# Kernel tuning notes

Hardware: AMD Instinct MI355X
Metric: run time of the kernel (lower is better)

Reference implementation:

```python
import jax, jax.numpy as jnp
import numpy as np

V = 8000      # output_size (vocab)
EMB = 256     # emb_size
ENC = 512     # enc_hid_size
DEC = 512     # dec_hid_size
HE = 20       # energizer hidden (fixed in source)


def setup_inputs() -> dict:
    key = jax.random.key(0)
    ks = jax.random.split(key, 12)
    B, S, T = 64, 128, 128
    s = 0.05
    return {
        "enc_hid": jax.random.normal(ks[0], (B, S, ENC), dtype=jnp.float32),
        "real_output": jax.random.randint(ks[1], (B, T), 0, V),
        "W_e1": jax.random.normal(ks[2], (ENC + DEC, HE), dtype=jnp.float32) * s,
        "b_e1": jnp.zeros((HE,), jnp.float32),
        "W_e2": jax.random.normal(ks[3], (HE, 1), dtype=jnp.float32) * s,
        "b_e2": jnp.zeros((1,), jnp.float32),
        "emb": jax.random.normal(ks[4], (V, EMB), dtype=jnp.float32) * s,
        "W_rnn": jax.random.normal(ks[5], (EMB + DEC + ENC, DEC), dtype=jnp.float32) * s,
        "b_rnn": jnp.zeros((DEC,), jnp.float32),
        "W_out": jax.random.normal(ks[6], (EMB + DEC + ENC, V), dtype=jnp.float32) * s,
        "b_out": jnp.zeros((V,), jnp.float32),
    }


def _decode(enc_hid, real_output, W_e1, b_e1, W_e2, b_e2, emb, W_rnn, b_rnn, W_out, b_out):
    B, S, _ = enc_hid.shape

    def step(carry, y_i):
        last_char, last_hidden = carry  # [B] int, [B,DEC]
        # additive attention, vectorized over all encoder positions
        hid_b = jnp.broadcast_to(last_hidden[:, None, :], (B, S, DEC))
        cat = jnp.concatenate([enc_hid, hid_b], axis=-1)          # [B,S,ENC+DEC]
        e = jax.nn.elu(cat @ W_e1 + b_e1)                          # [B,S,HE]
        e = jax.nn.elu(e @ W_e2 + b_e2)[..., 0]                    # [B,S]
        ew = jnp.exp(e)
        w = ew / jnp.sum(ew, axis=1, keepdims=True)                # [B,S]
        context = jnp.einsum('bs,bse->be', w, enc_hid)             # [B,ENC]
        last_ch = emb[last_char % V]                               # [B,EMB]
        new_hidden = jax.nn.elu(
            jnp.concatenate([last_ch, last_hidden, context], axis=1) @ W_rnn + b_rnn)
        out = jax.nn.elu(
            jnp.concatenate([last_ch, new_hidden, context], axis=1) @ W_out + b_out)
        # teacher_forcing_prob = 1.0 -> next char is the ground truth token
        return (y_i, new_hidden), (out, w)

    init = (jnp.zeros((B,), real_output.dtype), jnp.zeros((B, DEC), enc_hid.dtype))
    _, (outs, weights) = jax.lax.scan(step, init, real_output.T)   # [T,B,V], [T,B,S]
    return outs.transpose(1, 0, 2), weights.transpose(1, 0, 2)


def reference(enc_hid, real_output, W_e1, b_e1, W_e2, b_e2, emb, W_rnn, b_rnn, W_out, b_out):
    return _decode(enc_hid, real_output, W_e1, b_e1, W_e2, b_e2, emb,
                   W_rnn, b_rnn, W_out, b_out)
```

## Files before the change

kernel.cpp:

```cpp
#include <hip/hip_runtime.h>
#include <hip/hip_bf16.h>
#include <stdint.h>

#define BATCH 64
#define SLEN 128
#define TLEN 128
#define ENCD 512
#define DECD 512
#define EMBD 256
#define VOC  8000
#define HE   20
#define KX   1280
#define NPAD 8064

typedef __attribute__((ext_vector_type(8))) short short8;
typedef __attribute__((ext_vector_type(8))) _Float16 half8v;
typedef __attribute__((ext_vector_type(4))) float f32x4;
typedef _Float16 h2 __attribute__((ext_vector_type(2)));

__device__ inline unsigned short f2bf(float f) {
  union { float f; uint32_t u; } v; v.f = f;
  uint32_t r = v.u + 0x7fff + ((v.u >> 16) & 1);
  return (unsigned short)(r >> 16);
}
__device__ inline unsigned short f16bits(float f) {
  union { _Float16 h; unsigned short u; } c; c.h = (_Float16)f; return c.u;
}
__device__ inline uint32_t pkh2(float a, float b) {
  union { h2 h; uint32_t u; } v;
  v.h = h2{(_Float16)a, (_Float16)b};
  return v.u;
}
__device__ inline float fdot2(uint32_t a, uint32_t b, float c) {
#if __has_builtin(__builtin_amdgcn_fdot2)
  union { uint32_t u; h2 h; } x, y; x.u = a; y.u = b;
  return __builtin_amdgcn_fdot2(x.h, y.h, c, false);
#else
  union { uint32_t u; h2 h; } x, y; x.u = a; y.u = b;
  return c + (float)x.h[0] * (float)y.h[0] + (float)x.h[1] * (float)y.h[1];
#endif
}
__device__ inline float eluf(float x) { return x > 0.f ? x : (expf(x) - 1.f); }

typedef const __attribute__((address_space(1))) unsigned int* gptr_t;
typedef __attribute__((address_space(3))) unsigned int* lptr_t;
__device__ inline void gload16(const void* g, void* l) {
  __builtin_amdgcn_global_load_lds((gptr_t)g, (lptr_t)l, 16, 0, 0);
}

__global__ __launch_bounds__(256) void k_e1(const float* __restrict__ enc,
                                            const float* __restrict__ We1,
                                            float* __restrict__ E1) {
  __shared__ float rowbuf[4][ENCD];
  __shared__ float part[4][HE][2];
  int r0 = blockIdx.x * 4;
  int tid = threadIdx.x;
  for (int i = tid; i < 4 * ENCD; i += 256) {
    int rl = i >> 9, e = i & 511;
    rowbuf[rl][e] = enc[(size_t)(r0 + rl) * ENCD + e];
  }
  __syncthreads();
  if (tid < 160) {
    int kg = tid / 80, rem = tid % 80, rl = rem / 20, h = rem % 20;
    float acc = 0.f;
    for (int k = kg * 256; k < kg * 256 + 256; ++k)
      acc += rowbuf[rl][k] * We1[k * HE + h];
    part[rl][h][kg] = acc;
  }
  __syncthreads();
  if (tid < 80) {
    int rl = tid / 20, h = tid % 20;
    int r = r0 + rl, bb = r >> 7, ss = r & 127;
    E1[((size_t)bb * HE + h) * SLEN + ss] = part[rl][h][0] + part[rl][h][1];
  }
}

__global__ __launch_bounds__(256) void k_tr_wout(const float* __restrict__ Wo,
                                                 unsigned short* __restrict__ WoT) {
  __shared__ float tile[64][65];
  int n0 = blockIdx.x * 64, k0 = blockIdx.y * 64;
  int tid = threadIdx.x;
  for (int i = tid; i < 4096; i += 256) {
    int kk = i >> 6, nn = i & 63;
    int n = n0 + nn;
    tile[kk][nn] = (n < VOC) ? Wo[(size_t)(k0 + kk) * VOC + n] : 0.f;
  }
  __syncthreads();
  for (int i = tid; i < 4096; i += 256) {
    int nn = i >> 6, kk = i & 63;
    WoT[(size_t)(n0 + nn) * KX + k0 + kk] = f2bf(tile[kk][nn]);
  }
}

__global__ __launch_bounds__(256) void k_tr_w(const float* __restrict__ src,
                                              unsigned short* __restrict__ dst,
                                              int k0, int KN, int fmt) {
  __shared__ float tile[64][65];
  int n0 = blockIdx.x * 64, kt = blockIdx.y * 64;
  int tid = threadIdx.x;
  for (int i = tid; i < 4096; i += 256) {
    int kk = i >> 6, nn = i & 63;
    tile[kk][nn] = src[(size_t)(k0 + kt + kk) * 512 + n0 + nn];
  }
  __syncthreads();
  for (int i = tid; i < 4096; i += 256) {
    int nn = i >> 6, kk = i & 63;
    float v = tile[kk][nn];
    dst[(size_t)(n0 + nn) * KN + kt + kk] = fmt ? f2bf(v) : f16bits(v);
  }
}

__global__ __launch_bounds__(256) void k_prep_wr(const float* __restrict__ Wr,
                                                 unsigned short* __restrict__ W2) {
  int i = blockIdx.x * 256 + threadIdx.x;
  int n = i & 511;
  int j = (i >> 9) & 7;
  int kc = (i >> 12) & 31;
  int h = (i >> 17) & 1;
  int k = h * 256 + kc * 8 + j;
  W2[(((size_t)(h * 32 + kc) * 512) + n) * 8 + j] = f16bits(Wr[(size_t)(256 + k) * 512 + n]);
}

__global__ __launch_bounds__(256) void k_ench(const float* __restrict__ enc,
                                              unsigned short* __restrict__ ench) {
  int i = (blockIdx.x * 256 + threadIdx.x) * 4;
  float4 v = *(const float4*)(enc + i);
  ushort4 o = { f16bits(v.x), f16bits(v.y), f16bits(v.z), f16bits(v.w) };
  *(ushort4*)(ench + i) = o;
}

__global__ __launch_bounds__(256) void k_wh(const float* __restrict__ wout,
                                            unsigned short* __restrict__ wh) {
  int i = (blockIdx.x * 256 + threadIdx.x) * 4;
  float4 v = *(const float4*)(wout + i);
  ushort4 o = { f16bits(v.x), f16bits(v.y), f16bits(v.z), f16bits(v.w) };
  *(ushort4*)(wh + i) = o;
}

__global__ __launch_bounds__(256) void k_tr_encb(const float* __restrict__ enc,
                                                 unsigned short* __restrict__ encT) {
  __shared__ float tile[64][65];
  int b = blockIdx.x, e0 = blockIdx.y * 64, s0 = blockIdx.z * 64;
  int tid = threadIdx.x;
  const float* eb = enc + (size_t)b * SLEN * ENCD;
  for (int i = tid; i < 4096; i += 256) {
    int ss = i >> 6, ee = i & 63;
    tile[ss][ee] = eb[(size_t)(s0 + ss) * ENCD + e0 + ee];
  }
  __syncthreads();
  unsigned short* ob = encT + (size_t)b * ENCD * SLEN;
  for (int i = tid; i < 4096; i += 256) {
    int ee = i >> 6, ss = i & 63;
    ob[(size_t)(e0 + ee) * SLEN + s0 + ss] = f16bits(tile[ss][ee]);
  }
}

__global__ __launch_bounds__(256) void k_lc(const int* __restrict__ ro,
                                            const float* __restrict__ emb,
                                            unsigned short* __restrict__ X) {
  int r = blockIdx.x;
  int t = r >> 6, b = r & 63;
  int lc = (t == 0) ? 0 : ro[b * TLEN + t - 1];
  lc = ((lc % VOC) + VOC) % VOC;
  X[(size_t)r * KX + threadIdx.x] = f2bf(emb[(size_t)lc * EMBD + threadIdx.x]);
}

#define BM 128
#define BN 128
#define BK 64

template<int MODE>
__global__ __launch_bounds__(256) void k_gs(
    const unsigned short* __restrict__ A,
    const unsigned short* __restrict__ B,
    const float* __restrict__ bias,
    unsigned short* __restrict__ Cout)
{
  constexpr int As = (MODE == 0) ? KX : (MODE == 1 ? 512 : 128);
  constexpr int Bs = (MODE == 0) ? 256 : (MODE == 1 ? 512 : 128);
  constexpr int KT = (MODE == 0) ? 4 : (MODE == 1 ? 8 : 2);
  __shared__ __align__(16) unsigned short Asd[BM * BK];
  __shared__ __align__(16) unsigned short Bsd[BN * BK];
  int bx = blockIdx.x, by = blockIdx.y;
  int tid = threadIdx.x;
  int wid = tid >> 6, lane = tid & 63;
  int wr = wid >> 1, wc = wid & 1;

  f32x4 acc[4][4];
  for (int i = 0; i < 4; ++i)
    for (int j = 0; j < 4; ++j) acc[i][j] = (f32x4)0.f;

  const unsigned short* Abase = A + (size_t)by * BM * As;
  const unsigned short* Bbase = B + (size_t)bx * BN * Bs + (MODE == 2 ? (size_t)by * 512 * 128 : 0);

  for (int kt = 0; kt < KT; ++kt) {
    for (int j = 0; j < 4; ++j) {
      int c = tid + j * 256;
      int r = c >> 3, c16 = c & 7;
      int sk = c16 ^ (r & 7);
      gload16(Abase + (size_t)r * As + kt * BK + sk * 8, (char*)Asd + c * 16);
      gload16(Bbase + (size_t)r * Bs + kt * BK + sk * 8, (char*)Bsd + c * 16);
    }
    __syncthreads();
    for (int ks = 0; ks < 2; ++ks) {
      short8 af[4], bf[4];
      int kc = ks * 4 + (lane >> 4);
      for (int i = 0; i < 4; ++i) {
        int r = wr * 64 + i * 16 + (lane & 15);
        af[i] = *(const short8*)((const char*)Asd + r * 128 + ((kc ^ (r & 7)) * 16));
      }
      for (int j = 0; j < 4; ++j) {
        int r = wc * 64 + j * 16 + (lane & 15);
        bf[j] = *(const short8*)((const char*)Bsd + r * 128 + ((kc ^ (r & 7)) * 16));
      }
      for (int i = 0; i < 4; ++i)
        for (int j = 0; j < 4; ++j) {
          if constexpr (MODE == 0)
            acc[i][j] = __builtin_amdgcn_mfma_f32_16x16x32_bf16(af[i], bf[j], acc[i][j], 0, 0, 0);
          else
            acc[i][j] = __builtin_amdgcn_mfma_f32_16x16x32_f16(
                __builtin_bit_cast(half8v, af[i]), __builtin_bit_cast(half8v, bf[j]), acc[i][j], 0, 0, 0);
        }
    }
    __syncthreads();
  }

  int rl = lane >> 4, cl = lane & 15;
  for (int j = 0; j < 4; ++j) {
    int gn = bx * BN + wc * 64 + j * 16 + cl;
    for (int i = 0; i < 4; ++i) {
      for (int q = 0; q < 4; ++q) {
        int gm = by * BM + wr * 64 + i * 16 + rl * 4 + q;
        float v = acc[i][j][q];
        if constexpr (MODE == 0) {
          Cout[(size_t)gm * 512 + gn] = f16bits(v + bias[gn]);
        } else if constexpr (MODE == 1) {
          int bb = gm >> 7, s = gm & 127;
          Cout[(((size_t)(bb * 16 + (s >> 3)) * 512) + gn) * 8 + (s & 7)] = f16bits(v);
        } else {
          int tt = gm & 127, bb = gm >> 7;
          Cout[((size_t)tt * 64 + bb) * KX + 768 + gn] = f2bf(v);
        }
      }
    }
  }
}

#define STREAM4(PH) { \
  float a0 = 0, a1 = 0, a2 = 0, a3 = 0; \
  uint4 cb[8], nb[8]; \
  _Pragma("unroll") \
  for (int j = 0; j < 8; ++j) cb[j] = Wp[(size_t)j * 512]; \
  for (int blk = 0; blk < 4; ++blk) { \
    if (blk + 1 < 4) { \
      _Pragma("unroll") \
      for (int j = 0; j < 8; ++j) nb[j] = Wp[(size_t)((blk + 1) * 8 + j) * 512]; \
    } \
    _Pragma("unroll") \
    for (int j = 0; j < 8; ++j) { \
      uint4 wv = cb[j]; uint4 xv = hp4[hbase + blk * 8 + j]; \
      a0 = fdot2(wv.x, xv.x, a0); a1 = fdot2(wv.y, xv.y, a1); \
      a2 = fdot2(wv.z, xv.z, a2); a3 = fdot2(wv.w, xv.w, a3); \
    } \
    _Pragma("unroll") \
    for (int j = 0; j < 8; ++j) cb[j] = nb[j]; \
  } \
  ph[PH][mn] = (a0 + a1) + (a2 + a3); }

__global__ __launch_bounds__(1024) void k_recur(
    const float* __restrict__ We1,
    const float* __restrict__ be1,
    const float* __restrict__ We2,
    const float* __restrict__ be2,
    const uint4* __restrict__ W2,
    const uint4* __restrict__ encW2,
    const unsigned short* __restrict__ Remb,
    const float* __restrict__ E1g,
    unsigned short* __restrict__ X,
    float* __restrict__ wout)
{
  __shared__ __align__(16) uint4 el[16][512];
  __shared__ uint32_t E1p[HE][SLEN / 2];
  __shared__ uint32_t w1p[HE][257];
  __shared__ uint32_t hpair[DECD / 2];
  __shared__ uint32_t wpairS[SLEN / 2];
  __shared__ float ph[2][DECD];
  __shared__ float be1s[HE], w2s[HE];
  __shared__ float be2s;

  int b = blockIdx.x, tid = threadIdx.x;

  for (int i = tid; i < 16 * 512; i += 1024) ((uint4*)el)[i] = encW2[(size_t)b * 8192 + i];
  for (int i = tid; i < HE * (SLEN / 2); i += 1024) {
    int h = i >> 6, p = i & 63;
    const float* ebase = E1g + ((size_t)b * HE + h) * SLEN;
    ((uint32_t*)E1p)[i] = pkh2(ebase[2 * p], ebase[2 * p + 1]);
  }
  for (int i = tid; i < HE * 256; i += 1024) {
    int h = i >> 8, p = i & 255;
    w1p[h][p] = pkh2(We1[(size_t)(ENCD + 2 * p) * HE + h],
                     We1[(size_t)(ENCD + 2 * p + 1) * HE + h]);
  }
  for (int i = tid; i < DECD / 2; i += 1024) hpair[i] = 0;
  for (int i = tid; i < DECD; i += 1024) { ph[0][i] = 0.f; ph[1][i] = 0.f; }
  if (tid < HE) { be1s[tid] = be1[tid]; w2s[tid] = We2[tid]; }
  if (tid == 0) be2s = be2[0];
  __syncthreads();

  const int lane = tid & 63;
  const int wv_ = tid >> 6;
  int mn, mh0;
  if (tid < 448)      { mn = tid;        mh0 = 0; }
  else if (tid < 896) { mn = tid - 448;  mh0 = 1; }
  else if (tid < 960) { mn = 448 + lane; mh0 = 0; }
  else                { mn = 448 + lane; mh0 = 1; }
  const uint4* Wp = W2 + (size_t)(mh0 * 32) * 512 + mn;
  const uint4* hp4 = (const uint4*)hpair;
  const int hbase = mh0 * 32;

  int ah = lane % 20, aseg = lane / 20;
  int q0 = aseg * 86;
  int q1 = (aseg == 2) ? 256 : q0 + 86;
  if (aseg >= 3) { q0 = 0; q1 = 0; }

  for (int t = 0; t < TLEN; ++t) {
    const int rowr = t * BATCH + b;
    float rpre = 0.f;

    if (wv_ < 15) {
      if (tid < 512) {
        union { unsigned short u; _Float16 f; } c;
        c.u = Remb[(size_t)rowr * 512 + tid];
        rpre = (float)c.f;
      }
      STREAM4(mh0)
    } else {
      __builtin_amdgcn_s_setprio(1);
      float p0 = 0, p1 = 0;
      for (int q = q0; q < q1; q += 2) {
        p0 = fdot2(w1p[ah][q], hpair[q], p0);
        p1 = fdot2(w1p[ah][q + 1], hpair[q + 1], p1);
      }
      float p = p0 + p1;
      float pa = __shfl(p, lane + 20);
      float pb = __shfl(p, lane + 40);
      float edv = p + pa + pb + ((lane < HE) ? be1s[lane] : 0.f);
      float e0a = 0.f, e1a = 0.f;
      #pragma unroll
      for (int h = 0; h < HE; ++h) {
        union { uint32_t u; h2 hh; } e; e.u = E1p[h][lane];
        float ed = __shfl(edv, h);
        e0a += eluf((float)e.hh[0] + ed) * w2s[h];
        e1a += eluf((float)e.hh[1] + ed) * w2s[h];
      }
      float s0 = expf(eluf(e0a + be2s));
      float s1 = expf(eluf(e1a + be2s));
      float tot = s0 + s1;
      #pragma unroll
      for (int o = 1; o < 64; o <<= 1) tot += __shfl_xor(tot, o);
      float inv = 1.f / tot;
      float w0 = s0 * inv, w1 = s1 * inv;
      wpairS[lane] = pkh2(w0, w1);
      float2 wv2 = { w0, w1 };
      *(float2*)(wout + ((size_t)b * TLEN + t) * SLEN + 2 * lane) = wv2;
      __builtin_amdgcn_s_setprio(0);
      STREAM4(1)
    }
    __syncthreads();

    if (tid < 512) {
      int n = tid;
      float c0 = 0, c1 = 0, c2 = 0, c3 = 0;
      #pragma unroll
      for (int g = 0; g < 16; ++g) {
        uint4 ev = el[g][n];
        uint4 wv = ((const uint4*)wpairS)[g];
        c0 = fdot2(ev.x, wv.x, c0); c1 = fdot2(ev.y, wv.y, c1);
        c2 = fdot2(ev.z, wv.z, c2); c3 = fdot2(ev.w, wv.w, c3);
      }
      float v = rpre + ph[0][n] + ph[1][n] + (c0 + c1) + (c2 + c3);
      float aa = eluf(v);
      X[(size_t)rowr * KX + 256 + n] = f2bf(aa);
      float bb = __shfl_down(aa, 1);
      if (!(n & 1)) hpair[n >> 1] = pkh2(aa, bb);
    }
    __syncthreads();
  }
}

__global__ __launch_bounds__(256) void k_gemm(
    const unsigned short* __restrict__ Xb,
    const unsigned short* __restrict__ WoT,
    const float* __restrict__ bout,
    float* __restrict__ out)
{
  __shared__ __align__(16) unsigned short As[BM * BK];
  __shared__ __align__(16) unsigned short Bs[BN * BK];
  int bid = blockIdx.x;
  int swz = (bid & 7) * 504 + (bid >> 3);
  int bx = swz % 63;
  int by = swz / 63;
  int tid = threadIdx.x;
  int wid = tid >> 6, lane = tid & 63;
  int wr = wid >> 1, wc = wid & 1;

  f32x4 acc[4][4];
  for (int i = 0; i < 4; ++i)
    for (int j = 0; j < 4; ++j) acc[i][j] = (f32x4)0.f;

  const unsigned short* Abase = Xb + (size_t)by * BM * KX;
  const unsigned short* Bbase = WoT + (size_t)bx * BN * KX;

  for (int kt = 0; kt < KX / BK; ++kt) {
    for (int j = 0; j < 4; ++j) {
      int c = tid + j * 256;
      int r = c >> 3, c16 = c & 7;
      int sk = c16 ^ (r & 7);
      gload16(Abase + (size_t)r * KX + kt * BK + sk * 8, (char*)As + c * 16);
      gload16(Bbase + (size_t)r * KX + kt * BK + sk * 8, (char*)Bs + c * 16);
    }
    __syncthreads();
    for (int ks = 0; ks < 2; ++ks) {
      short8 af[4], bf[4];
      int kc = ks * 4 + (lane >> 4);
      for (int i = 0; i < 4; ++i) {
        int r = wr * 64 + i * 16 + (lane & 15);
        af[i] = *(const short8*)((const char*)As + r * 128 + ((kc ^ (r & 7)) * 16));
      }
      for (int j = 0; j < 4; ++j) {
        int r = wc * 64 + j * 16 + (lane & 15);
        bf[j] = *(const short8*)((const char*)Bs + r * 128 + ((kc ^ (r & 7)) * 16));
      }
      for (int i = 0; i < 4; ++i)
        for (int j = 0; j < 4; ++j)
          acc[i][j] = __builtin_amdgcn_mfma_f32_16x16x32_bf16(af[i], bf[j], acc[i][j], 0, 0, 0);
    }
    __syncthreads();
  }

  int rl = lane >> 4, cl = lane & 15;
  for (int j = 0; j < 4; ++j) {
    int gn = bx * BN + wc * 64 + j * 16 + cl;
    if (gn >= VOC) continue;
    float bv = bout[gn];
    for (int i = 0; i < 4; ++i) {
      for (int q = 0; q < 4; ++q) {
        int gm = by * BM + wr * 64 + i * 16 + rl * 4 + q;
        int tt = gm >> 6, bb = gm & 63;
        float v = acc[i][j][q] + bv;
        v = v > 0.f ? v : (expf(v) - 1.f);
        out[((size_t)bb * TLEN + tt) * VOC + gn] = v;
      }
    }
  }
}

extern "C" void kernel_launch(void* const* d_in, const int* in_sizes, int n_in,
                              void* d_out, int out_size, void* d_ws, size_t ws_size,
                              hipStream_t stream) {
  const float* enc  = (const float*)d_in[0];
  const int*   ro   = (const int*)d_in[1];
  const float* We1  = (const float*)d_in[2];
  const float* be1  = (const float*)d_in[3];
  const float* We2  = (const float*)d_in[4];
  const float* be2  = (const float*)d_in[5];
  const float* emb  = (const float*)d_in[6];
  const float* Wr   = (const float*)d_in[7];
  const float* brnn = (const float*)d_in[8];
  const float* Wo   = (const float*)d_in[9];
  const float* bo   = (const float*)d_in[10];

  char* ws = (char*)d_ws;
  unsigned short* X     = (unsigned short*)(ws);
  unsigned short* WoT   = (unsigned short*)(ws + 20971520);
  unsigned short* W2    = (unsigned short*)(ws + 41615360);
  unsigned short* WembT = (unsigned short*)(ws + 42139648);
  unsigned short* WctxT = (unsigned short*)(ws + 42401792);
  unsigned short* ench  = (unsigned short*)(ws + 42926080);
  float*          E1    = (float*)(ws + 51314688);
  unsigned short* Remb  = (unsigned short*)(ws + 51970048);
  unsigned short* encW2 = (unsigned short*)(ws + 60358656);
  unsigned short* encTh = ench;
  unsigned short* wh    = Remb;

  float* outs = (float*)d_out;
  float* wout = (float*)d_out + (size_t)BATCH * TLEN * VOC;

  k_lc     <<<dim3(8192),     256, 0, stream>>>(ro, emb, X);
  k_e1     <<<dim3(2048),     256, 0, stream>>>(enc, We1, E1);
  k_tr_wout<<<dim3(126, 20),  256, 0, stream>>>(Wo, WoT);
  k_tr_w   <<<dim3(8, 4),     256, 0, stream>>>(Wr, WembT, 0, 256, 1);
  k_tr_w   <<<dim3(8, 8),     256, 0, stream>>>(Wr, WctxT, 768, 512, 0);
  k_prep_wr<<<dim3(1024),     256, 0, stream>>>(Wr, W2);
  k_ench   <<<dim3(4096),     256, 0, stream>>>(enc, ench);
  k_gs<0>  <<<dim3(4, 64),    256, 0, stream>>>(X, WembT, brnn, Remb);
  k_gs<1>  <<<dim3(4, 64),    256, 0, stream>>>(ench, WctxT, brnn, encW2);
  k_recur  <<<dim3(64),      1024, 0, stream>>>(We1, be1, We2, be2,
                                                (const uint4*)W2, (const uint4*)encW2,
                                                Remb, E1, X, wout);
  k_wh     <<<dim3(1024),     256, 0, stream>>>(wout, wh);
  k_tr_encb<<<dim3(64, 8, 2), 256, 0, stream>>>(enc, encTh);
  k_gs<2>  <<<dim3(4, 64),    256, 0, stream>>>(wh, encTh, brnn, X);
  k_gemm   <<<dim3(4032),     256, 0, stream>>>(X, WoT, bo, outs);
  (void)in_sizes; (void)n_in; (void)out_size; (void)ws_size;
}
```

Before: 1.307 ms.

## Fuse prep kernels and overlap weight transposes with recurrent kernel blocks

The small preprocessing kernels are merged into two launches that branch on block index: embedding gather, encoder fp16 conversion and E1 in one, and the W_rnn transposes and repacks in the other. The W_out transpose and the encoder transpose no longer run as separate kernels. They now run in extra blocks of the recurrent kernel, which otherwise keeps only 64 workgroups busy on a GPU with many idle CUs, so this work overlaps the serial recurrence instead of adding to the critical path. The cost is a larger recurrent grid that may contend with the 64 recurrence blocks for memory bandwidth. It also relies on those 64 blocks being dispatched first.

After: 1.256 ms. 1.04x faster.

```diff
diff --git a/kernel.cpp b/kernel.cpp
--- a/kernel.cpp
+++ b/kernel.cpp
@@ -48,85 +48,81 @@
   __builtin_amdgcn_global_load_lds((gptr_t)g, (lptr_t)l, 16, 0, 0);
 }
 
-__global__ __launch_bounds__(256) void k_e1(const float* __restrict__ enc,
-                                            const float* __restrict__ We1,
-                                            float* __restrict__ E1) {
+__global__ __launch_bounds__(256) void k_pre1(const int* __restrict__ ro,
+                                              const float* __restrict__ emb,
+                                              unsigned short* __restrict__ X,
+                                              const float* __restrict__ enc,
+                                              unsigned short* __restrict__ ench,
+                                              const float* __restrict__ We1,
+                                              float* __restrict__ E1) {
   __shared__ float rowbuf[4][ENCD];
   __shared__ float part[4][HE][2];
-  int r0 = blockIdx.x * 4;
-  int tid = threadIdx.x;
-  for (int i = tid; i < 4 * ENCD; i += 256) {
-    int rl = i >> 9, e = i & 511;
-    rowbuf[rl][e] = enc[(size_t)(r0 + rl) * ENCD + e];
-  }
-  __syncthreads();
-  if (tid < 160) {
-    int kg = tid / 80, rem = tid % 80, rl = rem / 20, h = rem % 20;
-    float acc = 0.f;
-    for (int k = kg * 256; k < kg * 256 + 256; ++k)
-      acc += rowbuf[rl][k] * We1[k * HE + h];
-    part[rl][h][kg] = acc;
-  }
-  __syncthreads();
-  if (tid < 80) {
-    int rl = tid / 20, h = tid % 20;
-    int r = r0 + rl, bb = r >> 7, ss = r & 127;
-    E1[((size_t)bb * HE + h) * SLEN + ss] = part[rl][h][0] + part[rl][h][1];
-  }
-}
-
-__global__ __launch_bounds__(256) void k_tr_wout(const float* __restrict__ Wo,
-                                                 unsigned short* __restrict__ WoT) {
+  int bid = blockIdx.x, tid = threadIdx.x;
+  if (bid < 8192) {
+    int r = bid;
+    int t = r >> 6, b = r & 63;
+    int lc = (t == 0) ? 0 : ro[b * TLEN + t - 1];
+    lc = ((lc % VOC) + VOC) % VOC;
+    X[(size_t)r * KX + tid] = f2bf(emb[(size_t)lc * EMBD + tid]);
+  } else if (bid < 12288) {
+    int i = ((bid - 8192) * 256 + tid) * 4;
+    float4 v = *(const float4*)(enc + i);
+    ushort4 o = { f16bits(v.x), f16bits(v.y), f16bits(v.z), f16bits(v.w) };
+    *(ushort4*)(ench + i) = o;
+  } else {
+    int r0 = (bid - 12288) * 4;
+    for (int i = tid; i < 4 * ENCD; i += 256) {
+      int rl = i >> 9, e = i & 511;
+      rowbuf[rl][e] = enc[(size_t)(r0 + rl) * ENCD + e];
+    }
+    __syncthreads();
+    if (tid < 160) {
+      int kg = tid / 80, rem = tid % 80, rl = rem / 20, h = rem % 20;
+      float acc = 0.f;
+      for (int k = kg * 256; k < kg * 256 + 256; ++k)
+        acc += rowbuf[rl][k] * We1[k * HE + h];
+      part[rl][h][kg] = acc;
+    }
+    __syncthreads();
+    if (tid < 80) {
+      int rl = tid / 20, h = tid % 20;
+      int r = r0 + rl, bb = r >> 7, ss = r & 127;
+      E1[((size_t)bb * HE + h) * SLEN + ss] = part[rl][h][0] + part[rl][h][1];
+    }
+  }
+}
+
+__global__ __launch_bounds__(256) void k_pre2(const float* __restrict__ Wr,
+                                              unsigned short* __restrict__ WembT,
+                                              unsigned short* __restrict__ WctxT,
+                                              unsigned short* __restrict__ W2) {
   __shared__ float tile[64][65];
-  int n0 = blockIdx.x * 64, k0 = blockIdx.y * 64;
-  int tid = threadIdx.x;
-  for (int i = tid; i < 4096; i += 256) {
-    int kk = i >> 6, nn = i & 63;
-    int n = n0 + nn;
-    tile[kk][nn] = (n < VOC) ? Wo[(size_t)(k0 + kk) * VOC + n] : 0.f;
-  }
-  __syncthreads();
-  for (int i = tid; i < 4096; i += 256) {
-    int nn = i >> 6, kk = i & 63;
-    WoT[(size_t)(n0 + nn) * KX + k0 + kk] = f2bf(tile[kk][nn]);
-  }
-}
-
-__global__ __launch_bounds__(256) void k_tr_w(const float* __restrict__ src,
-                                              unsigned short* __restrict__ dst,
-                                              int k0, int KN, int fmt) {
-  __shared__ float tile[64][65];
-  int n0 = blockIdx.x * 64, kt = blockIdx.y * 64;
-  int tid = threadIdx.x;
-  for (int i = tid; i < 4096; i += 256) {
-    int kk = i >> 6, nn = i & 63;
-    tile[kk][nn] = src[(size_t)(k0 + kt + kk) * 512 + n0 + nn];
-  }
-  __syncthreads();
-  for (int i = tid; i < 4096; i += 256) {
-    int nn = i >> 6, kk = i & 63;
-    float v = tile[kk][nn];
-    dst[(size_t)(n0 + nn) * KN + kt + kk] = fmt ? f2bf(v) : f16bits(v);
-  }
-}
-
-__global__ __launch_bounds__(256) void k_prep_wr(const float* __restrict__ Wr,
-                                                 unsigned short* __restrict__ W2) {
-  int i = blockIdx.x * 256 + threadIdx.x;
-  int n = i & 511;
-  int j = (i >> 9) & 7;
-  int kc = (i >> 12) & 31;
-  int h = (i >> 17) & 1;
-  int k = h * 256 + kc * 8 + j;
-  W2[(((size_t)(h * 32 + kc) * 512) + n) * 8 + j] = f16bits(Wr[(size_t)(256 + k) * 512 + n]);
-}
-
-__global__ __launch_bounds__(256) void k_ench(const float* __restrict__ enc,
-                                              unsigned short* __restrict__ ench) {
-  int i = (blockIdx.x * 256 + threadIdx.x) * 4;
-  float4 v = *(const float4*)(enc + i);
-  ushort4 o = { f16bits(v.x), f16bits(v.y), f16bits(v.z), f16bits(v.w) };
-  *(ushort4*)(ench + i) = o;
+  int bid = blockIdx.x, tid = threadIdx.x;
+  if (bid < 96) {
+    int k0, KN, fmt, bx, by;
+    unsigned short* dst;
+    if (bid < 32) { k0 = 0;   KN = 256; fmt = 1; bx = bid & 7; by = bid >> 3; dst = WembT; }
+    else          { int id2 = bid - 32; k0 = 768; KN = 512; fmt = 0; bx = id2 & 7; by = id2 >> 3; dst = WctxT; }
+    int n0 = bx * 64, kt = by * 64;
+    for (int i = tid; i < 4096; i += 256) {
+      int kk = i >> 6, nn = i & 63;
+      tile[kk][nn] = Wr[(size_t)(k0 + kt + kk) * 512 + n0 + nn];
+    }
+    __syncthreads();
+    for (int i = tid; i < 4096; i += 256) {
+      int nn = i >> 6, kk = i & 63;
+      float v = tile[kk][nn];
+      dst[(size_t)(n0 + nn) * KN + kt + kk] = fmt ? f2bf(v) : f16bits(v);
+    }
+  } else {
+    int i = (bid - 96) * 256 + tid;
+    int n = i & 511;
+    int j = (i >> 9) & 7;
+    int kc = (i >> 12) & 31;
+    int h = (i >> 17) & 1;
+    int k = h * 256 + kc * 8 + j;
+    W2[(((size_t)(h * 32 + kc) * 512) + n) * 8 + j] = f16bits(Wr[(size_t)(256 + k) * 512 + n]);
+  }
 }
 
 __global__ __launch_bounds__(256) void k_wh(const float* __restrict__ wout,
@@ -135,34 +131,6 @@
   float4 v = *(const float4*)(wout + i);
   ushort4 o = { f16bits(v.x), f16bits(v.y), f16bits(v.z), f16bits(v.w) };
   *(ushort4*)(wh + i) = o;
-}
-
-__global__ __launch_bounds__(256) void k_tr_encb(const float* __restrict__ enc,
-                                                 unsigned short* __restrict__ encT) {
-  __shared__ float tile[64][65];
-  int b = blockIdx.x, e0 = blockIdx.y * 64, s0 = blockIdx.z * 64;
-  int tid = threadIdx.x;
-  const float* eb = enc + (size_t)b * SLEN * ENCD;
-  for (int i = tid; i < 4096; i += 256) {
-    int ss = i >> 6, ee = i & 63;
-    tile[ss][ee] = eb[(size_t)(s0 + ss) * ENCD + e0 + ee];
-  }
-  __syncthreads();
-  unsigned short* ob = encT + (size_t)b * ENCD * SLEN;
-  for (int i = tid; i < 4096; i += 256) {
-    int ee = i >> 6, ss = i & 63;
-    ob[(size_t)(e0 + ee) * SLEN + s0 + ss] = f16bits(tile[ss][ee]);
-  }
-}
-
-__global__ __launch_bounds__(256) void k_lc(const int* __restrict__ ro,
-                                            const float* __restrict__ emb,
-                                            unsigned short* __restrict__ X) {
-  int r = blockIdx.x;
-  int t = r >> 6, b = r & 63;
-  int lc = (t == 0) ? 0 : ro[b * TLEN + t - 1];
-  lc = ((lc % VOC) + VOC) % VOC;
-  X[(size_t)r * KX + threadIdx.x] = f2bf(emb[(size_t)lc * EMBD + threadIdx.x]);
 }
 
 #define BM 128
@@ -277,7 +245,11 @@
     const unsigned short* __restrict__ Remb,
     const float* __restrict__ E1g,
     unsigned short* __restrict__ X,
-    float* __restrict__ wout)
+    float* __restrict__ wout,
+    const float* __restrict__ Wo,
+    unsigned short* __restrict__ WoT,
+    const float* __restrict__ enc,
+    unsigned short* __restrict__ encTh)
 {
   __shared__ __align__(16) uint4 el[16][512];
   __shared__ uint32_t E1p[HE][SLEN / 2];
@@ -288,7 +260,50 @@
   __shared__ float be1s[HE], w2s[HE];
   __shared__ float be2s;
 
-  int b = blockIdx.x, tid = threadIdx.x;
+  int bid = blockIdx.x, tid = threadIdx.x;
+
+  if (bid >= 64) {
+    float (*tile)[65] = (float(*)[65])el;
+    if (bid < 694) {
+      for (int q = 0; q < 4; ++q) {
+        int t4 = (bid - 64) * 4 + q;
+        int n0 = (t4 % 126) * 64, k0 = (t4 / 126) * 64;
+        for (int i = tid; i < 4096; i += 1024) {
+          int kk = i >> 6, nn = i & 63;
+          int n = n0 + nn;
+          tile[kk][nn] = (n < VOC) ? Wo[(size_t)(k0 + kk) * VOC + n] : 0.f;
+        }
+        __syncthreads();
+        for (int i = tid; i < 4096; i += 1024) {
+          int nn = i >> 6, kk = i & 63;
+          WoT[(size_t)(n0 + nn) * KX + k0 + kk] = f2bf(tile[kk][nn]);
+        }
+        __syncthreads();
+      }
+    } else {
+      for (int q = 0; q < 4; ++q) {
+        int t4 = (bid - 694) * 4 + q;
+        int eb_ = t4 >> 4;
+        int e0 = ((t4 >> 1) & 7) * 64;
+        int s0 = (t4 & 1) * 64;
+        const float* ebp = enc + (size_t)eb_ * SLEN * ENCD;
+        for (int i = tid; i < 4096; i += 1024) {
+          int ss = i >> 6, ee = i & 63;
+          tile[ss][ee] = ebp[(size_t)(s0 + ss) * ENCD + e0 + ee];
+        }
+        __syncthreads();
+        unsigned short* ob = encTh + (size_t)eb_ * ENCD * SLEN;
+        for (int i = tid; i < 4096; i += 1024) {
+          int ee = i >> 6, ss = i & 63;
+          ob[(size_t)(e0 + ee) * SLEN + s0 + ss] = f16bits(tile[ss][ee]);
+        }
+        __syncthreads();
+      }
+    }
+    return;
+  }
+
+  int b = bid;
 
   for (int i = tid; i < 16 * 512; i += 1024) ((uint4*)el)[i] = encW2[(size_t)b * 8192 + i];
   for (int i = tid; i < HE * (SLEN / 2); i += 1024) {
@@ -486,21 +501,16 @@
   float* outs = (float*)d_out;
   float* wout = (float*)d_out + (size_t)BATCH * TLEN * VOC;
 
-  k_lc     <<<dim3(8192),     256, 0, stream>>>(ro, emb, X);
-  k_e1     <<<dim3(2048),     256, 0, stream>>>(enc, We1, E1);
-  k_tr_wout<<<dim3(126, 20),  256, 0, stream>>>(Wo, WoT);
-  k_tr_w   <<<dim3(8, 4),     256, 0, stream>>>(Wr, WembT, 0, 256, 1);
-  k_tr_w   <<<dim3(8, 8),     256, 0, stream>>>(Wr, WctxT, 768, 512, 0);
-  k_prep_wr<<<dim3(1024),     256, 0, stream>>>(Wr, W2);
-  k_ench   <<<dim3(4096),     256, 0, stream>>>(enc, ench);
-  k_gs<0>  <<<dim3(4, 64),    256, 0, stream>>>(X, WembT, brnn, Remb);
-  k_gs<1>  <<<dim3(4, 64),    256, 0, stream>>>(ench, WctxT, brnn, encW2);
-  k_recur  <<<dim3(64),      1024, 0, stream>>>(We1, be1, We2, be2,
-                                                (const uint4*)W2, (const uint4*)encW2,
-                                                Remb, E1, X, wout);
-  k_wh     <<<dim3(1024),     256, 0, stream>>>(wout, wh);
-  k_tr_encb<<<dim3(64, 8, 2), 256, 0, stream>>>(enc, encTh);
-  k_gs<2>  <<<dim3(4, 64),    256, 0, stream>>>(wh, encTh, brnn, X);
-  k_gemm   <<<dim3(4032),     256, 0, stream>>>(X, WoT, bo, outs);
+  k_pre1 <<<dim3(14336),  256, 0, stream>>>(ro, emb, X, enc, ench, We1, E1);
+  k_pre2 <<<dim3(1120),   256, 0, stream>>>(Wr, WembT, WctxT, W2);
+  k_gs<0><<<dim3(4, 64),  256, 0, stream>>>(X, WembT, brnn, Remb);
+  k_gs<1><<<dim3(4, 64),  256, 0, stream>>>(ench, WctxT, brnn, encW2);
+  k_recur<<<dim3(950),   1024, 0, stream>>>(We1, be1, We2, be2,
+                                            (const uint4*)W2, (const uint4*)encW2,
+                                            Remb, E1, X, wout,
+                                            Wo, WoT, enc, encTh);
+  k_wh   <<<dim3(1024),   256, 0, stream>>>(wout, wh);
+  k_gs<2><<<dim3(4, 64),  256, 0, stream>>>(wh, encTh, brnn, X);
+  k_gemm <<<dim3(4032),   256, 0, stream>>>(X, WoT, bo, outs);
   (void)in_sizes; (void)n_in; (void)out_size; (void)ws_size;
 }
```
